# Kernel optimization log

Hardware: AMD Instinct MI355X
Metric: run time of the kernel (lower is better)

## Reference

```python
import jax, jax.numpy as jnp
import numpy as np

HEADS = 16

def setup_inputs() -> dict:
    key = jax.random.key(0)
    k1, k2, k3 = jax.random.split(key, 3)
    B, E, W = 4, 1024, 2048
    x = jax.random.normal(k1, (B, E, W), dtype=jnp.float32)
    # dense Linear params (bias=True): M ~ randn * ((E+E)/2)^-0.5, b ~ randn / E^2
    M_d = jax.random.normal(k2, (E, E), dtype=jnp.float32) * (E ** -0.5)
    b_d = jax.random.normal(k3, (E,), dtype=jnp.float32) / (E ** 2)
    return {"x": x, "M_d": M_d, "b_d": b_d}


def reference(x, M_d, b_d):
    B, E, W = x.shape
    H = HEADS
    D = E // H
    # NOTE: original code computes self.linear(x) but discards it (KQV = x.view)
    kqv = x.reshape(B, H, D, W)  # [B,H,D,W]
    # scores[b,h,i,j] = sum_d kqv[b,h,d,i]*kqv[b,h,d,j], scaled by E^-0.5
    scores = jnp.einsum('bhdi,bhdj->bhij', kqv, kqv) * (E ** -0.5)
    # causal_factor = tril(ones, diagonal=-1): mask strictly-lower (i>j) to -inf
    i = jnp.arange(W)[:, None]
    j = jnp.arange(W)[None, :]
    scores = jnp.where(i > j, -jnp.inf, scores)
    # softmax over axis -2 (over i, per column j)
    att = jax.nn.softmax(scores, axis=-2)  # [B,H,W,W]
    t = jnp.einsum('bhdi,bhij->bhdj', kqv, att)  # [B,H,D,W]
    t = t.reshape(B, E, W)
    # dense Linear: (B,W,E) @ M + b, transposed back to (B,E,W)
    out = jnp.einsum('bew,ef->bfw', t, M_d) + b_d[None, :, None]
    return out
```

## Files before the change

### kernel.cpp

```cpp
#include <hip/hip_runtime.h>
#include <hip/hip_bf16.h>

constexpr int B  = 4;
constexpr int E  = 1024;
constexpr int Wn = 2048;
constexpr int H  = 16;
constexpr int Dh = 64;

typedef short bf16x8 __attribute__((ext_vector_type(8)));
typedef float f32x4  __attribute__((ext_vector_type(4)));

__device__ inline unsigned short f2bf(float f){
    unsigned int u = __builtin_bit_cast(unsigned int, f);
    u = (u + 0x7fffu + ((u >> 16) & 1u)) >> 16;
    return (unsigned short)u;
}
__device__ inline float bf2f(unsigned short u){
    return __builtin_bit_cast(float, (unsigned int)u << 16);
}
__device__ inline unsigned int pack_bf16_trunc(float lo, float hi){
    return __builtin_amdgcn_perm(__builtin_bit_cast(unsigned int, hi),
                                 __builtin_bit_cast(unsigned int, lo), 0x07060302u);
}
__device__ inline float exp2_fast(float x){ return __builtin_amdgcn_exp2f(x); }
__device__ inline int SW(int c){ return c ^ (((c >> 5) & 7) << 2); }

#define GLDS(g, l) __builtin_amdgcn_global_load_lds( \
    (const __attribute__((address_space(1))) void*)(g), \
    (__attribute__((address_space(3))) void*)(l), 16, 0, 0)

__device__ __constant__ signed char SBT[40] =
    {3,4,5,6,7,7,8,8,9,9,10,10,11,11,11,12,12,12,13,13,13,14,14,14,15,15,15,15,
     2,6,10,14, 1,5,9,13, 0,4,8,12};
__device__ __constant__ signed char CHT[40] =
    {0,0,0,0,0,1,0,1,0,1,0,1,0,1,2,0,1,2,0,1,2,0,1,2,0,1,2,3,
     0,1,2,3, 0,1,2,3, 0,1,2,3};
__device__ __constant__ signed char BASET[16] =
    {0,1,2,3,4,6,8,10,12,15,18,21,24,28,32,36};

__global__ __launch_bounds__(256) void k_prep(const float* __restrict__ x,
                                              unsigned short* __restrict__ xS,
                                              unsigned short* __restrict__ xdi){
    __shared__ float tile[64*257];
    const float cs = 0.2123304349f;
    const int t  = threadIdx.x;
    const int bh = blockIdx.x >> 3;
    const int w0 = (blockIdx.x & 7) << 8;

    {
        const int r = t >> 2, seg = t & 3;
        const float* src = x + ((size_t)bh*64 + r)*Wn + w0 + seg*64;
        float* dst = tile + r*257;
        #pragma unroll
        for (int i = 0; i < 16; ++i){
            float4 v = *reinterpret_cast<const float4*>(src + i*4);
            int c0 = seg*64 + i*4;
            dst[SW(c0+0)] = v.x; dst[SW(c0+1)] = v.y;
            dst[SW(c0+2)] = v.z; dst[SW(c0+3)] = v.w;
        }
    }
    __syncthreads();

    {
        const int kgw = t & 3, g = (t >> 2) & 7, r0 = t >> 5;
        #pragma unroll
        for (int rr = 0; rr < 8; ++rr){
            const int r = r0*8 + rr;
            const float* base = tile + r*257;
            const int c0 = g*32 + 4*kgw;
            union { unsigned short us[8]; uint4 v; } u;
            #pragma unroll
            for (int j2 = 0; j2 < 4; ++j2){
                u.us[j2]   = f2bf(base[SW(c0 + j2)]);
                u.us[4+j2] = f2bf(base[SW(c0 + 16 + j2)]);
            }
            *reinterpret_cast<uint4*>(xdi + ((size_t)bh*64 + r)*Wn + w0 + g*32 + 8*kgw) = u.v;
        }
    }
    {
        const int w = t;
        #pragma unroll
        for (int dg = 0; dg < 8; ++dg){
            union { unsigned short us[8]; uint4 v; } u;
            #pragma unroll
            for (int i = 0; i < 8; ++i)
                u.us[i] = f2bf(tile[(dg*8 + i)*257 + SW(w)] * cs);
            *reinterpret_cast<uint4*>(xS + ((size_t)bh*Wn + w0 + w)*64 + dg*8) = u.v;
        }
    }
}

__global__ void k_MT(const float* __restrict__ M, unsigned short* __restrict__ MT){
    int tid = blockIdx.x*256 + threadIdx.x;
    int f  = tid & (E-1);
    int eg = tid >> 10;
    union { unsigned short us[8]; uint4 v; } u;
    #pragma unroll
    for (int i = 0; i < 8; i++) u.us[i] = f2bf(M[(size_t)(eg*8+i)*E + f]);
    *reinterpret_cast<uint4*>(MT + (size_t)f*E + eg*8) = u.v;
}

__global__ __launch_bounds__(256)
void k_attn(const unsigned short* __restrict__ xS,
            const unsigned short* __restrict__ xdi,
            unsigned short* __restrict__ pacc,
            float* __restrict__ pl){
    __shared__ char Klds[2*8192];
    __shared__ char Vlds[2*8192];

    const int lane = threadIdx.x & 63;
    const int wv   = threadIdx.x >> 6;
    const int jl = lane & 15, kg = lane >> 4;
    const int sw = jl & 7;

    const int p    = blockIdx.x;
    const int xcd  = p & 7;
    const int q    = p >> 3;
    const int hh   = q & 7;
    const int widx = q >> 3;
    const int bh   = xcd*8 + hh;

    const int sb  = SBT[widx];
    const int ch  = CHT[widx];
    const int nst = min(8, (sb+1)*2 - ch*8);
    const int kvb = ch*512;
    const bool isLast = (kvb + nst*64 == (sb+1)*128);

    const int q0w = sb*128 + wv*32;

    const bf16x8* xSr = reinterpret_cast<const bf16x8*>(xS + (size_t)bh*Wn*Dh);
    bf16x8 bq[2][2];
    #pragma unroll
    for (int jt = 0; jt < 2; jt++){
        bq[jt][0] = xSr[(q0w + jt*16 + jl)*8 + kg];
        bq[jt][1] = xSr[(q0w + jt*16 + jl)*8 + 4 + kg];
    }
    union { bf16x8 v; unsigned short us[8]; } ones;
    #pragma unroll
    for (int i2 = 0; i2 < 8; i2++) ones.us[i2] = 0x3F80;

    f32x4 acc[2][4] = {};
    f32x4 accl[2] = {};

    const char* Kg = (const char*)xS  + (size_t)bh*Wn*128;
    const char* Vg = (const char*)xdi + (size_t)bh*Dh*(Wn*2);
    const int rloc = 8*wv + (lane >> 3);
    const int ksw  = ((lane & 7) ^ (rloc & 7))*16;

    auto STAGE = [&](int buf, int kvT){
        char* Kb = Klds + buf*8192;
        char* Vb = Vlds + buf*8192;
        const char* kg0 = Kg + (size_t)(kvT + rloc)*128 + ksw;
        const char* vg0 = Vg + (size_t)rloc*(Wn*2) + kvT*2 + ksw;
        GLDS(kg0,             Kb + wv*1024);
        GLDS(kg0 + 32*128,    Kb + 4096 + wv*1024);
        GLDS(vg0,             Vb + wv*1024);
        GLDS(vg0 + (size_t)32*(Wn*2), Vb + 4096 + wv*1024);
    };

    auto computeS = [&](int buf, int s, bool dg){
        const char* Kb = Klds + buf*8192;
        const char* Vb = Vlds + buf*8192;
        const int r0 = s*32 + jl, r1 = r0 + 16;
        bf16x8 k0a = *(const bf16x8*)(Kb + r0*128 + ((kg    )^sw)*16);
        bf16x8 k0b = *(const bf16x8*)(Kb + r0*128 + ((kg + 4)^sw)*16);
        bf16x8 k1a = *(const bf16x8*)(Kb + r1*128 + ((kg    )^sw)*16);
        bf16x8 k1b = *(const bf16x8*)(Kb + r1*128 + ((kg + 4)^sw)*16);
        const int vsw = ((s*4 + kg)^sw)*16;
        bf16x8 v0 = *(const bf16x8*)(Vb + (     jl)*128 + vsw);
        bf16x8 v1 = *(const bf16x8*)(Vb + (16 + jl)*128 + vsw);
        bf16x8 v2 = *(const bf16x8*)(Vb + (32 + jl)*128 + vsw);
        bf16x8 v3 = *(const bf16x8*)(Vb + (48 + jl)*128 + vsw);

        #pragma unroll
        for (int jt = 0; jt < 2; jt++){
            f32x4 s0 = {0,0,0,0}, s1 = {0,0,0,0};
            s0 = __builtin_amdgcn_mfma_f32_16x16x32_bf16(k0a, bq[jt][0], s0, 0,0,0);
            s0 = __builtin_amdgcn_mfma_f32_16x16x32_bf16(k0b, bq[jt][1], s0, 0,0,0);
            s1 = __builtin_amdgcn_mfma_f32_16x16x32_bf16(k1a, bq[jt][0], s1, 0,0,0);
            s1 = __builtin_amdgcn_mfma_f32_16x16x32_bf16(k1b, bq[jt][1], s1, 0,0,0);

            union { bf16x8 v; unsigned int w[4]; } bp;
            if (!dg){
                bp.w[0] = pack_bf16_trunc(exp2_fast(s0[0]), exp2_fast(s0[1]));
                bp.w[1] = pack_bf16_trunc(exp2_fast(s0[2]), exp2_fast(s0[3]));
                bp.w[2] = pack_bf16_trunc(exp2_fast(s1[0]), exp2_fast(s1[1]));
                bp.w[3] = pack_bf16_trunc(exp2_fast(s1[2]), exp2_fast(s1[3]));
            } else {
                const int lim = 16*jt + jl;
                float pp[8];
                #pragma unroll
                for (int r = 0; r < 4; r++){
                    int c = 4*kg + r;
                    pp[r]   = (c      <= lim) ? exp2_fast(s0[r]) : 0.f;
                    pp[4+r] = (c + 16 <= lim) ? exp2_fast(s1[r]) : 0.f;
                }
                bp.w[0] = pack_bf16_trunc(pp[0], pp[1]);
                bp.w[1] = pack_bf16_trunc(pp[2], pp[3]);
                bp.w[2] = pack_bf16_trunc(pp[4], pp[5]);
                bp.w[3] = pack_bf16_trunc(pp[6], pp[7]);
            }
            accl[jt] = __builtin_amdgcn_mfma_f32_16x16x32_bf16(ones.v, bp.v, accl[jt], 0,0,0);
            acc[jt][0] = __builtin_amdgcn_mfma_f32_16x16x32_bf16(v0, bp.v, acc[jt][0], 0,0,0);
            acc[jt][1] = __builtin_amdgcn_mfma_f32_16x16x32_bf16(v1, bp.v, acc[jt][1], 0,0,0);
            acc[jt][2] = __builtin_amdgcn_mfma_f32_16x16x32_bf16(v2, bp.v, acc[jt][2], 0,0,0);
            acc[jt][3] = __builtin_amdgcn_mfma_f32_16x16x32_bf16(v3, bp.v, acc[jt][3], 0,0,0);
        }
    };

    STAGE(0, kvb);
    for (int t = 0; t < nst; ++t){
        const int kvT = kvb + 64*t;
        if (t + 1 < nst){
            STAGE((t+1)&1, kvT + 64);
            asm volatile("s_waitcnt vmcnt(4)" ::: "memory");
        } else {
            asm volatile("s_waitcnt vmcnt(0)" ::: "memory");
        }
        __builtin_amdgcn_s_barrier();
        __builtin_amdgcn_sched_barrier(0);
        #pragma unroll
        for (int s = 0; s < 2; ++s){
            const int kv = kvT + 32*s;
            if (kv > q0w) continue;
            computeS(t & 1, s, isLast && (kv == q0w));
        }
        asm volatile("s_waitcnt lgkmcnt(0)" ::: "memory");
        __builtin_amdgcn_sched_barrier(0);
        __builtin_amdgcn_s_barrier();
    }

    const int slot = bh*40 + BASET[sb] + ch;
    if (kg == 0){
        pl[(size_t)slot*128 + wv*32 + jl]      = accl[0][0];
        pl[(size_t)slot*128 + wv*32 + 16 + jl] = accl[1][0];
    }
    unsigned short* pa = pacc + (size_t)slot*8192;
    #pragma unroll
    for (int jt = 0; jt < 2; jt++){
        #pragma unroll
        for (int dt = 0; dt < 4; dt++){
            union { unsigned short us[4]; ushort4 v; } o;
            #pragma unroll
            for (int r = 0; r < 4; r++) o.us[r] = f2bf(acc[jt][dt][r]);
            *reinterpret_cast<ushort4*>(pa + (wv*32 + jt*16 + jl)*64 + dt*16 + 4*kg) = o.v;
        }
    }
}

__global__ __launch_bounds__(256) void k_reduce(const unsigned short* __restrict__ pacc,
                                                const float* __restrict__ pl,
                                                unsigned short* __restrict__ tws){
    const int g  = blockIdx.x;
    const int bh = g >> 4, sb = g & 15;
    const int t  = threadIdx.x;
    const int qq = t >> 1;
    const int db = (t & 1)*32;
    const int nch   = (sb + 4) >> 2;
    const int slot0 = bh*40 + BASET[sb];

    float l = 0.f;
    float a[32];
    #pragma unroll
    for (int i = 0; i < 32; ++i) a[i] = 0.f;
    for (int c = 0; c < nch; ++c){
        l += pl[(size_t)(slot0 + c)*128 + qq];
        const unsigned short* pa = pacc + (size_t)(slot0 + c)*8192 + qq*64 + db;
        #pragma unroll
        for (int i = 0; i < 4; ++i){
            union { uint4 v; unsigned short us[8]; } r0;
            r0.v = *reinterpret_cast<const uint4*>(pa + i*8);
            #pragma unroll
            for (int j2 = 0; j2 < 8; ++j2) a[i*8 + j2] += bf2f(r0.us[j2]);
        }
    }
    const float inv = 1.0f / l;
    unsigned short* tw = tws + ((size_t)(bh >> 4)*Wn + sb*128 + qq)*E + (bh & 15)*Dh + db;
    #pragma unroll
    for (int i = 0; i < 4; ++i){
        union { uint4 v; unsigned short us[8]; } o;
        #pragma unroll
        for (int j2 = 0; j2 < 8; ++j2) o.us[j2] = f2bf(a[i*8 + j2] * inv);
        *reinterpret_cast<uint4*>(tw + i*8) = o.v;
    }
}

__global__ __launch_bounds__(256)
void k_gemm(const unsigned short* __restrict__ MT,
            const unsigned short* __restrict__ tws,
            const float* __restrict__ bd,
            float* __restrict__ out){
    __shared__ char Alds[2*16384];
    __shared__ char Blds[2*16384];

    const int lane = threadIdx.x & 63;
    const int wv   = threadIdx.x >> 6;
    const int jl = lane & 15, kg = lane >> 4;
    const int sw = jl & 7;

    const int p   = blockIdx.x;
    const int blk = (p & 7)*64 + (p >> 3);
    const int b  = blk >> 7;
    const int t2 = blk & 127;
    const int fblk = (t2 >> 4)*128;
    const int wblk = (t2 & 15)*128;
    const int f0 = fblk + (wv >> 1)*64;
    const int w0 = wblk + (wv &  1)*64;

    const char* Ag = (const char*)MT + (size_t)fblk*E*2;
    const char* Bg = (const char*)tws + ((size_t)b*Wn + wblk)*E*2;
    const int rloc = 8*wv + (lane >> 3);
    const int scw  = ((lane & 7) ^ (lane >> 3))*16;

    auto STAGE = [&](int buf, int e0){
        char* Ab = Alds + buf*16384;
        char* Bb = Blds + buf*16384;
        const char* ag = Ag + (size_t)rloc*(E*2) + e0*2 + scw;
        const char* bg = Bg + (size_t)rloc*(E*2) + e0*2 + scw;
        #pragma unroll
        for (int g = 0; g < 4; ++g){
            GLDS(ag + (size_t)g*32*(E*2), Ab + g*4096 + wv*1024);
            GLDS(bg + (size_t)g*32*(E*2), Bb + g*4096 + wv*1024);
        }
    };

    f32x4 acc[4][4] = {};

    auto COMP = [&](int buf){
        const char* Ab = Alds + buf*16384 + ((wv >> 1)*64)*128;
        const char* Bb = Blds + buf*16384 + ((wv &  1)*64)*128;
        #pragma unroll
        for (int h = 0; h < 2; ++h){
            const int cs = ((h*4 + kg) ^ sw)*16;
            bf16x8 am[4], bn[4];
            #pragma unroll
            for (int i = 0; i < 4; i++) am[i] = *(const bf16x8*)(Ab + (i*16 + jl)*128 + cs);
            #pragma unroll
            for (int j = 0; j < 4; j++) bn[j] = *(const bf16x8*)(Bb + (j*16 + jl)*128 + cs);
            #pragma unroll
            for (int i = 0; i < 4; i++)
                #pragma unroll
                for (int j = 0; j < 4; j++)
                    acc[i][j] = __builtin_amdgcn_mfma_f32_16x16x32_bf16(am[i], bn[j], acc[i][j], 0,0,0);
        }
    };

    STAGE(0, 0);
    for (int t = 0; t < 16; ++t){
        if (t < 15){
            STAGE((t+1)&1, (t+1)*64);
            asm volatile("s_waitcnt vmcnt(8)" ::: "memory");
        } else {
            asm volatile("s_waitcnt vmcnt(0)" ::: "memory");
        }
        __builtin_amdgcn_s_barrier();
        __builtin_amdgcn_sched_barrier(0);
        COMP(t & 1);
        asm volatile("s_waitcnt lgkmcnt(0)" ::: "memory");
        __builtin_amdgcn_sched_barrier(0);
        __builtin_amdgcn_s_barrier();
    }

    #pragma unroll
    for (int i = 0; i < 4; i++){
        float bias[4];
        #pragma unroll
        for (int r = 0; r < 4; r++) bias[r] = bd[f0 + i*16 + 4*kg + r];
        #pragma unroll
        for (int j = 0; j < 4; j++){
            #pragma unroll
            for (int r = 0; r < 4; r++){
                out[((size_t)b*E + f0 + i*16 + 4*kg + r)*Wn + w0 + j*16 + jl]
                    = acc[i][j][r] + bias[r];
            }
        }
    }
}

extern "C" void kernel_launch(void* const* d_in, const int* in_sizes, int n_in,
                              void* d_out, int out_size, void* d_ws, size_t ws_size,
                              hipStream_t stream) {
    const float* x  = (const float*)d_in[0];
    const float* Md = (const float*)d_in[1];
    const float* bd = (const float*)d_in[2];
    float* out = (float*)d_out;

    char* ws = (char*)d_ws;
    unsigned short* xS   = (unsigned short*)(ws);
    unsigned short* xdi  = (unsigned short*)(ws + (16u << 20));
    unsigned short* MT   = (unsigned short*)(ws + (32u << 20));
    unsigned short* tws  = (unsigned short*)(ws + (34u << 20));
    float*          pl   = (float*)(ws + (50u << 20));
    unsigned short* pacc = (unsigned short*)(ws + (52u << 20));

    hipLaunchKernelGGL(k_prep,   dim3(512),  dim3(256), 0, stream, x, xS, xdi);
    hipLaunchKernelGGL(k_MT,     dim3(512),  dim3(256), 0, stream, Md, MT);
    hipLaunchKernelGGL(k_attn,   dim3(2560), dim3(256), 0, stream, xS, xdi, pacc, pl);
    hipLaunchKernelGGL(k_reduce, dim3(1024), dim3(256), 0, stream, pacc, pl, tws);
    hipLaunchKernelGGL(k_gemm,   dim3(B*(E/128)*(Wn/128)), dim3(256), 0, stream, MT, tws, bd, out);
}
```

Measured before the change: 113.8 us.

## Use 512-thread attention blocks over 256-query tiles with new split-KV schedule

The attention kernel now runs 8 waves per block, each block covering 256 query rows instead of 128, with a new precomputed table of work items that splits the KV range into chunks of up to 12 stages. Blocks that cover a whole query tile normalize and write the output directly, so only split tiles go through the reduce kernel, which now launches fewer blocks. Each thread stages half as many loads because the larger block shares the copy work. The partial accumulators are placed in the output buffer as scratch space. This cuts block count, reduction traffic and per-thread load issue, but makes each block heavier and changes load balance across the causal triangle.

```diff
diff --git a/kernel.cpp b/kernel.cpp
--- a/kernel.cpp
+++ b/kernel.cpp
@@ -29,14 +29,18 @@
     (const __attribute__((address_space(1))) void*)(g), \
     (__attribute__((address_space(3))) void*)(l), 16, 0, 0)
 
-__device__ __constant__ signed char SBT[40] =
-    {3,4,5,6,7,7,8,8,9,9,10,10,11,11,11,12,12,12,13,13,13,14,14,14,15,15,15,15,
-     2,6,10,14, 1,5,9,13, 0,4,8,12};
-__device__ __constant__ signed char CHT[40] =
-    {0,0,0,0,0,1,0,1,0,1,0,1,0,1,2,0,1,2,0,1,2,0,1,2,0,1,2,3,
-     0,1,2,3, 0,1,2,3, 0,1,2,3};
-__device__ __constant__ signed char BASET[16] =
-    {0,1,2,3,4,6,8,10,12,15,18,21,24,28,32,36};
+__device__ __constant__ signed char SB2T[19] =
+    {2,1,3,3,5,5,5,7,7,7,7,4,4,6,6,6,6,4,0};
+__device__ __constant__ signed char KV64T[19] =
+    {0,0,0,8,0,8,16,0,8,16,24,0,7,0,7,14,21,14,0};
+__device__ __constant__ signed char NSTT[19] =
+    {12,8,8,8,8,8,8,8,8,8,8,7,7,7,7,7,7,6,4};
+__device__ __constant__ signed char SLOTT[19] =
+    {-1,-1,0,1,5,6,7,12,13,14,15,2,3,8,9,10,11,4,-1};
+__device__ __constant__ signed char LASTT[19] =
+    {1,1,0,1,0,0,1,0,0,0,1,0,0,0,0,0,1,1,1};
+__device__ __constant__ signed char NCHT[5]   = {2,3,3,4,4};
+__device__ __constant__ signed char SBASET[5] = {0,2,5,8,12};
 
 __global__ __launch_bounds__(256) void k_prep(const float* __restrict__ x,
                                               unsigned short* __restrict__ xS,
@@ -100,9 +104,10 @@
     *reinterpret_cast<uint4*>(MT + (size_t)f*E + eg*8) = u.v;
 }
 
-__global__ __launch_bounds__(256)
+__global__ __launch_bounds__(512)
 void k_attn(const unsigned short* __restrict__ xS,
             const unsigned short* __restrict__ xdi,
+            unsigned short* __restrict__ tws,
             unsigned short* __restrict__ pacc,
             float* __restrict__ pl){
     __shared__ char Klds[2*8192];
@@ -115,18 +120,17 @@
 
     const int p    = blockIdx.x;
     const int xcd  = p & 7;
-    const int q    = p >> 3;
-    const int hh   = q & 7;
-    const int widx = q >> 3;
+    const int hh   = (p >> 3) & 7;
+    const int widx = p >> 6;
     const int bh   = xcd*8 + hh;
 
-    const int sb  = SBT[widx];
-    const int ch  = CHT[widx];
-    const int nst = min(8, (sb+1)*2 - ch*8);
-    const int kvb = ch*512;
-    const bool isLast = (kvb + nst*64 == (sb+1)*128);
-
-    const int q0w = sb*128 + wv*32;
+    const int sb2  = SB2T[widx];
+    const int kvb  = (int)KV64T[widx] * 64;
+    const int nst  = NSTT[widx];
+    const int slot = SLOTT[widx];
+    const bool isLast = LASTT[widx] != 0;
+
+    const int q0w = sb2*256 + wv*32;
 
     const bf16x8* xSr = reinterpret_cast<const bf16x8*>(xS + (size_t)bh*Wn*Dh);
     bf16x8 bq[2][2];
@@ -148,14 +152,10 @@
     const int ksw  = ((lane & 7) ^ (rloc & 7))*16;
 
     auto STAGE = [&](int buf, int kvT){
-        char* Kb = Klds + buf*8192;
-        char* Vb = Vlds + buf*8192;
         const char* kg0 = Kg + (size_t)(kvT + rloc)*128 + ksw;
         const char* vg0 = Vg + (size_t)rloc*(Wn*2) + kvT*2 + ksw;
-        GLDS(kg0,             Kb + wv*1024);
-        GLDS(kg0 + 32*128,    Kb + 4096 + wv*1024);
-        GLDS(vg0,             Vb + wv*1024);
-        GLDS(vg0 + (size_t)32*(Wn*2), Vb + 4096 + wv*1024);
+        GLDS(kg0, Klds + buf*8192 + wv*1024);
+        GLDS(vg0, Vlds + buf*8192 + wv*1024);
     };
 
     auto computeS = [&](int buf, int s, bool dg){
@@ -213,7 +213,7 @@
         const int kvT = kvb + 64*t;
         if (t + 1 < nst){
             STAGE((t+1)&1, kvT + 64);
-            asm volatile("s_waitcnt vmcnt(4)" ::: "memory");
+            asm volatile("s_waitcnt vmcnt(2)" ::: "memory");
         } else {
             asm volatile("s_waitcnt vmcnt(0)" ::: "memory");
         }
@@ -230,42 +230,58 @@
         __builtin_amdgcn_s_barrier();
     }
 
-    const int slot = bh*40 + BASET[sb] + ch;
-    if (kg == 0){
-        pl[(size_t)slot*128 + wv*32 + jl]      = accl[0][0];
-        pl[(size_t)slot*128 + wv*32 + 16 + jl] = accl[1][0];
-    }
-    unsigned short* pa = pacc + (size_t)slot*8192;
-    #pragma unroll
-    for (int jt = 0; jt < 2; jt++){
-        #pragma unroll
-        for (int dt = 0; dt < 4; dt++){
-            union { unsigned short us[4]; ushort4 v; } o;
-            #pragma unroll
-            for (int r = 0; r < 4; r++) o.us[r] = f2bf(acc[jt][dt][r]);
-            *reinterpret_cast<ushort4*>(pa + (wv*32 + jt*16 + jl)*64 + dt*16 + 4*kg) = o.v;
-        }
-    }
-}
-
-__global__ __launch_bounds__(256) void k_reduce(const unsigned short* __restrict__ pacc,
+    if (slot < 0){
+        #pragma unroll
+        for (int jt = 0; jt < 2; jt++){
+            const float inv = 1.0f / accl[jt][0];
+            unsigned short* trow = tws + ((size_t)(bh >> 4)*Wn + q0w + jt*16 + jl)*E + (bh & 15)*Dh;
+            #pragma unroll
+            for (int dt = 0; dt < 4; dt++){
+                union { unsigned short us[4]; ushort4 v; } o;
+                #pragma unroll
+                for (int r = 0; r < 4; r++) o.us[r] = f2bf(acc[jt][dt][r] * inv);
+                *reinterpret_cast<ushort4*>(trow + dt*16 + 4*kg) = o.v;
+            }
+        }
+    } else {
+        const int gslot = bh*16 + slot;
+        if (kg == 0){
+            pl[(size_t)gslot*256 + wv*32 + jl]      = accl[0][0];
+            pl[(size_t)gslot*256 + wv*32 + 16 + jl] = accl[1][0];
+        }
+        unsigned short* pa = pacc + (size_t)gslot*16384;
+        #pragma unroll
+        for (int jt = 0; jt < 2; jt++){
+            #pragma unroll
+            for (int dt = 0; dt < 4; dt++){
+                union { unsigned short us[4]; ushort4 v; } o;
+                #pragma unroll
+                for (int r = 0; r < 4; r++) o.us[r] = f2bf(acc[jt][dt][r]);
+                *reinterpret_cast<ushort4*>(pa + (wv*32 + jt*16 + jl)*64 + dt*16 + 4*kg) = o.v;
+            }
+        }
+    }
+}
+
+__global__ __launch_bounds__(512) void k_reduce(const unsigned short* __restrict__ pacc,
                                                 const float* __restrict__ pl,
                                                 unsigned short* __restrict__ tws){
-    const int g  = blockIdx.x;
-    const int bh = g >> 4, sb = g & 15;
-    const int t  = threadIdx.x;
-    const int qq = t >> 1;
-    const int db = (t & 1)*32;
-    const int nch   = (sb + 4) >> 2;
-    const int slot0 = bh*40 + BASET[sb];
+    const int g   = blockIdx.x;
+    const int bh  = g / 5, s5 = g % 5;
+    const int sb2 = 3 + s5;
+    const int t   = threadIdx.x;
+    const int qq  = t >> 1;
+    const int db  = (t & 1)*32;
+    const int nch   = NCHT[s5];
+    const int slot0 = bh*16 + SBASET[s5];
 
     float l = 0.f;
     float a[32];
     #pragma unroll
     for (int i = 0; i < 32; ++i) a[i] = 0.f;
     for (int c = 0; c < nch; ++c){
-        l += pl[(size_t)(slot0 + c)*128 + qq];
-        const unsigned short* pa = pacc + (size_t)(slot0 + c)*8192 + qq*64 + db;
+        l += pl[(size_t)(slot0 + c)*256 + qq];
+        const unsigned short* pa = pacc + (size_t)(slot0 + c)*16384 + qq*64 + db;
         #pragma unroll
         for (int i = 0; i < 4; ++i){
             union { uint4 v; unsigned short us[8]; } r0;
@@ -275,7 +291,7 @@
         }
     }
     const float inv = 1.0f / l;
-    unsigned short* tw = tws + ((size_t)(bh >> 4)*Wn + sb*128 + qq)*E + (bh & 15)*Dh + db;
+    unsigned short* tw = tws + ((size_t)(bh >> 4)*Wn + sb2*256 + qq)*E + (bh & 15)*Dh + db;
     #pragma unroll
     for (int i = 0; i < 4; ++i){
         union { uint4 v; unsigned short us[8]; } o;
@@ -391,11 +407,11 @@
     unsigned short* MT   = (unsigned short*)(ws + (32u << 20));
     unsigned short* tws  = (unsigned short*)(ws + (34u << 20));
     float*          pl   = (float*)(ws + (50u << 20));
-    unsigned short* pacc = (unsigned short*)(ws + (52u << 20));
+    unsigned short* pacc = (unsigned short*)d_out;
 
     hipLaunchKernelGGL(k_prep,   dim3(512),  dim3(256), 0, stream, x, xS, xdi);
     hipLaunchKernelGGL(k_MT,     dim3(512),  dim3(256), 0, stream, Md, MT);
-    hipLaunchKernelGGL(k_attn,   dim3(2560), dim3(256), 0, stream, xS, xdi, pacc, pl);
-    hipLaunchKernelGGL(k_reduce, dim3(1024), dim3(256), 0, stream, pacc, pl, tws);
+    hipLaunchKernelGGL(k_attn,   dim3(19*64), dim3(512), 0, stream, xS, xdi, tws, pacc, pl);
+    hipLaunchKernelGGL(k_reduce, dim3(320),  dim3(512), 0, stream, pacc, pl, tws);
     hipLaunchKernelGGL(k_gemm,   dim3(B*(E/128)*(Wn/128)), dim3(256), 0, stream, MT, tws, bd, out);
 }
```

After: 109.5 us, median of 4. 1.04x faster.
